# Kernel tuning notes

Measured on AMD Instinct MI355X. Metric: run time of the kernel, lower is better.

The kernel has to match this reference:

```python
import jax, jax.numpy as jnp
import numpy as np

B, N, ND = 4096, 28, 3        # batch, nodes (2 hands x 14 joints), xyz
ED, DD = 512, 256             # encoder dim, decoder dim
H, DH = 8, 64                 # heads, dim_head (inner = 512)
EDEPTH, DDEPTH = 2, 1
EMLP, DMLP = 4 * ED, 4 * DD
NM = 14                       # num_masked = int(0.5 * 28)


def _ln(x, s, b):
    m = jnp.mean(x, -1, keepdims=True)
    v = jnp.var(x, -1, keepdims=True)
    return (x - m) * jax.lax.rsqrt(v + 1e-5) * s + b


def _transformer(x, a, ln1_s, ln1_b, Wqkv, Wo, bo, ln2_s, ln2_b, W1, b1, W2, b2):
    # pre-norm transformer; adjacency a [b,n,n] enters as an additive attention bias
    b, n, _ = x.shape
    scale = DH ** -0.5
    for i in range(ln1_s.shape[0]):
        h = _ln(x, ln1_s[i], ln1_b[i])
        q, k, v = jnp.split(h @ Wqkv[i], 3, axis=-1)
        q = q.reshape(b, n, H, DH).transpose(0, 2, 1, 3)
        k = k.reshape(b, n, H, DH).transpose(0, 2, 1, 3)
        v = v.reshape(b, n, H, DH).transpose(0, 2, 1, 3)
        dots = jnp.einsum('bhid,bhjd->bhij', q, k) * scale + a[:, None]
        attn = jax.nn.softmax(dots, axis=-1)
        o = jnp.einsum('bhij,bhjd->bhid', attn, v).transpose(0, 2, 1, 3).reshape(b, n, H * DH)
        x = x + o @ Wo[i] + bo[i]
        h2 = _ln(x, ln2_s[i], ln2_b[i])
        x = x + jax.nn.gelu(h2 @ W1[i] + b1[i]) @ W2[i] + b2[i]
    return x


def setup_inputs() -> dict:
    key = jax.random.key(0)
    ks = iter(jax.random.split(key, 40))
    nrm = lambda shp, s=0.02: jax.random.normal(next(ks), shp, dtype=jnp.float32) * s
    x = jax.random.normal(next(ks), (B, N, ND), dtype=jnp.float32)
    a = jax.random.uniform(next(ks), (B, N, N), dtype=jnp.float32)
    perm = jnp.argsort(jax.random.uniform(next(ks), (B, N)), axis=-1).astype(jnp.int32)
    masked_indices, unmasked_indices = perm[:, :NM], perm[:, NM:]
    inp = dict(x=x, a=a, masked_indices=masked_indices, unmasked_indices=unmasked_indices)
    inp.update(
        W_emb=nrm((ND, ED)), b_emb=jnp.zeros((ED,), jnp.float32), pos_emb=nrm((N, ED), 0.02),
        e_ln1_s=jnp.ones((EDEPTH, ED)), e_ln1_b=jnp.zeros((EDEPTH, ED)),
        e_Wqkv=nrm((EDEPTH, ED, 3 * H * DH)), e_Wo=nrm((EDEPTH, H * DH, ED)), e_bo=jnp.zeros((EDEPTH, ED)),
        e_ln2_s=jnp.ones((EDEPTH, ED)), e_ln2_b=jnp.zeros((EDEPTH, ED)),
        e_W1=nrm((EDEPTH, ED, EMLP)), e_b1=jnp.zeros((EDEPTH, EMLP)),
        e_W2=nrm((EDEPTH, EMLP, ED)), e_b2=jnp.zeros((EDEPTH, ED)),
        enc2dec_W=nrm((ED, DD)), enc2dec_b=jnp.zeros((DD,), jnp.float32),
        mask_token=nrm((DD,), 1.0), dec_pos_emb=nrm((N, DD), 0.02),
        d_ln1_s=jnp.ones((DDEPTH, DD)), d_ln1_b=jnp.zeros((DDEPTH, DD)),
        d_Wqkv=nrm((DDEPTH, DD, 3 * H * DH)), d_Wo=nrm((DDEPTH, H * DH, DD)), d_bo=jnp.zeros((DDEPTH, DD)),
        d_ln2_s=jnp.ones((DDEPTH, DD)), d_ln2_b=jnp.zeros((DDEPTH, DD)),
        d_W1=nrm((DDEPTH, DD, DMLP)), d_b1=jnp.zeros((DDEPTH, DMLP)),
        d_W2=nrm((DDEPTH, DMLP, DD)), d_b2=jnp.zeros((DDEPTH, DD)),
        pred_W=nrm((DD, ND)), pred_b=jnp.zeros((ND,), jnp.float32),
    )
    return inp


def reference(x, a, masked_indices, unmasked_indices,
              W_emb, b_emb, pos_emb,
              e_ln1_s, e_ln1_b, e_Wqkv, e_Wo, e_bo, e_ln2_s, e_ln2_b, e_W1, e_b1, e_W2, e_b2,
              enc2dec_W, enc2dec_b, mask_token, dec_pos_emb,
              d_ln1_s, d_ln1_b, d_Wqkv, d_Wo, d_bo, d_ln2_s, d_ln2_b, d_W1, d_b1, d_W2, d_b2,
              pred_W, pred_b):
    # node embedding (1x1 conv over nodes == per-node linear) + positional embedding
    tokens = x @ W_emb + b_emb + pos_emb                                   # [B,N,ED]
    unm_tok = jnp.take_along_axis(tokens, unmasked_indices[:, :, None], axis=1)  # [B,N-NM,ED]
    masked_nodes = jnp.take_along_axis(x, masked_indices[:, :, None], axis=1)    # [B,NM,ND]
    # batched adjacency slicing (replaces the per-sample python loop in torch)
    unmasked_a = jax.vmap(lambda ai, ii: ai[ii[:, None], ii[None, :]])(a, unmasked_indices)
    enc = _transformer(unm_tok, unmasked_a,
                       e_ln1_s, e_ln1_b, e_Wqkv, e_Wo, e_bo, e_ln2_s, e_ln2_b, e_W1, e_b1, e_W2, e_b2)
    dec_tok = enc @ enc2dec_W + enc2dec_b                                  # [B,N-NM,DD]
    mask_toks = mask_token + dec_pos_emb[masked_indices]                   # [B,NM,DD]
    # NOTE: faithful to original: unmasked pos-emb tokens are computed but NOT used in the cat
    decoder_tokens = jnp.concatenate([mask_toks, dec_tok], axis=1)         # [B,N,DD]
    decoded = _transformer(decoder_tokens, a,
                           d_ln1_s, d_ln1_b, d_Wqkv, d_Wo, d_bo, d_ln2_s, d_ln2_b, d_W1, d_b1, d_W2, d_b2)
    mt = jnp.take_along_axis(decoded, masked_indices[:, :, None], axis=1)  # [B,NM,DD]
    masked_pred = mt @ pred_W + pred_b                                     # [B,NM,ND]
    recon_loss = jnp.mean((masked_pred - masked_nodes) ** 2)
    return (decoder_tokens, masked_nodes, masked_indices, masked_pred, recon_loss)
```

## Files before the change

kernel.cpp:

```cpp
#include <hip/hip_runtime.h>
#include <math.h>

#define B_TOT 4096
#define N_SEQ 28
#define NDIM 3
#define ED 512
#define DD 256
#define NH 8
#define DHD 64
#define EMLP 2048
#define DMLP 1024
#define NM 14
#define NU 14

typedef __attribute__((ext_vector_type(8))) short short8;
typedef __attribute__((ext_vector_type(4))) float f32x4;
typedef unsigned short ushort_t;
typedef unsigned int uint_t;

__device__ __forceinline__ float gelu_f(float x) {
    float x3 = x * x * x;
    return 0.5f * x * (1.0f + tanhf(0.7978845608028654f * (x + 0.044715f * x3)));
}
__device__ __forceinline__ ushort_t f2bf(float f) {
    union { float f; uint_t u; } c; c.f = f;
    uint_t u = c.u;
    return (ushort_t)((u + 0x7FFFu + ((u >> 16) & 1u)) >> 16);
}
__device__ __forceinline__ float bf2f(ushort_t h) {
    union { uint_t u; float f; } c; c.u = ((uint_t)h) << 16;
    return c.f;
}
__device__ __forceinline__ float bf_lo(uint_t u) {
    union { uint_t u; float f; } c; c.u = u << 16;
    return c.f;
}
__device__ __forceinline__ float bf_hi(uint_t u) {
    union { uint_t u; float f; } c; c.u = u & 0xFFFF0000u;
    return c.f;
}
__device__ __forceinline__ void gl_lds16(const ushort_t* g, ushort_t* l) {
    __builtin_amdgcn_global_load_lds(
        (const __attribute__((address_space(1))) unsigned int*)g,
        (__attribute__((address_space(3))) unsigned int*)l, 16, 0, 0);
}

__global__ void k_zero(float* p) { p[threadIdx.x] = 0.0f; }
__global__ void k_final(const float* acc, float* out) {
    out[0] = acc[0] * (1.0f / (float)(B_TOT * NM * NDIM));
}

__global__ void k_wconv(const float* __restrict__ W, ushort_t* __restrict__ Wt, int K, int N) {
    __shared__ float tile[32][33];
    int n0 = blockIdx.x * 32, k0 = blockIdx.y * 32;
    int tr = threadIdx.x >> 5, tc = threadIdx.x & 31;
#pragma unroll
    for (int i = 0; i < 4; ++i)
        tile[tr + i * 8][tc] = W[(size_t)(k0 + tr + i * 8) * N + n0 + tc];
    __syncthreads();
#pragma unroll
    for (int i = 0; i < 4; ++i)
        Wt[(size_t)(n0 + tr + i * 8) * K + k0 + tc] = f2bf(tile[tc][tr + i * 8]);
}

__global__ void k_embed(const float* __restrict__ x, const float* __restrict__ a,
                        const int* __restrict__ mi, const int* __restrict__ ui,
                        const float* __restrict__ W_emb, const float* __restrict__ b_emb,
                        const float* __restrict__ pos_emb,
                        ushort_t* __restrict__ X, float* __restrict__ ua,
                        float* __restrict__ out_mn, float* __restrict__ out_midx,
                        int base) {
    int s = blockIdx.x;
    int g = base + s;
    int t = threadIdx.x;
    for (int i = 0; i < NU; ++i) {
        int u = ui[g * NU + i];
        float x0 = x[((size_t)g * N_SEQ + u) * NDIM + 0];
        float x1 = x[((size_t)g * N_SEQ + u) * NDIM + 1];
        float x2 = x[((size_t)g * N_SEQ + u) * NDIM + 2];
        for (int d = t; d < ED; d += 256) {
            X[((size_t)s * NU + i) * ED + d] = f2bf(
                x0 * W_emb[d] + x1 * W_emb[ED + d] + x2 * W_emb[2 * ED + d]
                + b_emb[d] + pos_emb[(size_t)u * ED + d]);
        }
    }
    for (int idx = t; idx < NU * NU; idx += 256) {
        int i = idx / NU, j = idx % NU;
        int uii = ui[g * NU + i], ujj = ui[g * NU + j];
        ua[(size_t)s * NU * NU + idx] = a[(size_t)g * N_SEQ * N_SEQ + (size_t)uii * N_SEQ + ujj];
    }
    for (int idx = t; idx < NM * NDIM; idx += 256) {
        int i = idx / NDIM, c = idx % NDIM;
        int m = mi[g * NM + i];
        out_mn[((size_t)g * NM + i) * NDIM + c] = x[((size_t)g * N_SEQ + m) * NDIM + c];
    }
    for (int i = t; i < NM; i += 256) {
        out_midx[(size_t)g * NM + i] = (float)mi[g * NM + i];
    }
}

template <int D>
__global__ void k_ln(const ushort_t* __restrict__ in, ushort_t* __restrict__ out,
                     const float* __restrict__ sc, const float* __restrict__ bi, int M) {
    int wave = threadIdx.x >> 6;
    int lane = threadIdx.x & 63;
    int row = blockIdx.x * 4 + wave;
    if (row >= M) return;
    constexpr int PL = D / 64;
    const ushort_t* rp = in + (size_t)row * D + lane * PL;
    uint_t u[PL / 2];
    if (PL == 8) *(uint4*)u = *(const uint4*)rp;
    else *(uint2*)u = *(const uint2*)rp;
    float v[PL];
    float sum = 0.f, sq = 0.f;
#pragma unroll
    for (int q = 0; q < PL / 2; ++q) {
        v[2 * q] = bf_lo(u[q]);
        v[2 * q + 1] = bf_hi(u[q]);
    }
#pragma unroll
    for (int j = 0; j < PL; ++j) { sum += v[j]; sq += v[j] * v[j]; }
#pragma unroll
    for (int o = 32; o >= 1; o >>= 1) {
        sum += __shfl_xor(sum, o);
        sq += __shfl_xor(sq, o);
    }
    float mean = sum * (1.0f / D);
    float var = sq * (1.0f / D) - mean * mean;
    float r = rsqrtf(var + 1e-5f);
    uint_t w[PL / 2];
#pragma unroll
    for (int q = 0; q < PL / 2; ++q) {
        int d = lane * PL + 2 * q;
        float a0 = (v[2 * q] - mean) * r * sc[d] + bi[d];
        float a1 = (v[2 * q + 1] - mean) * r * sc[d + 1] + bi[d + 1];
        w[q] = (uint_t)f2bf(a0) | ((uint_t)f2bf(a1) << 16);
    }
    ushort_t* op = out + (size_t)row * D + lane * PL;
    if (PL == 8) *(uint4*)op = *(uint4*)w;
    else *(uint2*)op = *(uint2*)w;
}

template <int ACT, int OM, int NTv>
__global__ __launch_bounds__(256) void k_gemm_mfma(
    const ushort_t* __restrict__ A, const ushort_t* __restrict__ Wt,
    const float* __restrict__ bias, const ushort_t* __restrict__ res,
    ushort_t* __restrict__ Cout, ushort_t* __restrict__ VTout, int M, int N, int K) {
    __shared__ ushort_t As[128 * 32];
    __shared__ ushort_t Bs[128 * 32];
    const int t = threadIdx.x;
    const int gx = gridDim.x;
    int flat = blockIdx.y * gx + blockIdx.x;
    int nwg = gx * gridDim.y;
    int q8 = nwg >> 3, r8 = nwg & 7;
    int xcd = flat & 7, loc = flat >> 3;
    int wg = (xcd < r8 ? xcd * (q8 + 1) : r8 * (q8 + 1) + (xcd - r8) * q8) + loc;
    const int bm = wg / gx, bn = wg % gx;

    const int lane = t & 63;
    const int wave = t >> 6;
    const int wr = wave >> 1, wc = wave & 1;
    const int l15 = lane & 15;
    const int kg = (lane >> 4) * 8;

    const int srow = wave * 32 + (lane >> 2);
    const int scol = (lane & 3) * 8;
    const ushort_t* Ag = A + (size_t)(bm * 128 + srow) * K + scol;
    const ushort_t* Bg = Wt + (size_t)(bn * 128 + srow) * K + scol;
    ushort_t* Al0 = &As[(wave * 32) * 32];
    ushort_t* Al1 = &As[(wave * 32 + 16) * 32];
    ushort_t* Bl0 = &Bs[(wave * 32) * 32];
    ushort_t* Bl1 = &Bs[(wave * 32 + 16) * 32];

    f32x4 acc[4][4] = {};

    for (int k0 = 0; k0 < K; k0 += 32) {
        gl_lds16(Ag + k0, Al0);
        gl_lds16(Ag + (size_t)16 * K + k0, Al1);
        gl_lds16(Bg + k0, Bl0);
        gl_lds16(Bg + (size_t)16 * K + k0, Bl1);
        __syncthreads();
        short8 af[4], bfr[4];
#pragma unroll
        for (int m = 0; m < 4; ++m)
            af[m] = *(const short8*)&As[(wr * 64 + m * 16 + l15) * 32 + kg];
#pragma unroll
        for (int n = 0; n < 4; ++n)
            bfr[n] = *(const short8*)&Bs[(wc * 64 + n * 16 + l15) * 32 + kg];
#pragma unroll
        for (int m = 0; m < 4; ++m)
#pragma unroll
            for (int n = 0; n < 4; ++n)
                acc[m][n] = __builtin_amdgcn_mfma_f32_16x16x32_bf16(af[m], bfr[n], acc[m][n], 0, 0, 0);
        __syncthreads();
    }

    const int crow0 = bm * 128 + wr * 64;
    const int ccol0 = bn * 128 + wc * 64;
#pragma unroll
    for (int m = 0; m < 4; ++m) {
#pragma unroll
        for (int n = 0; n < 4; ++n) {
            int col = ccol0 + n * 16 + l15;
            float bv = bias ? bias[col] : 0.0f;
#pragma unroll
            for (int r = 0; r < 4; ++r) {
                int row = crow0 + m * 16 + (lane >> 4) * 4 + r;
                float v = acc[m][n][r] + bv;
                if (res) v += bf2f(res[(size_t)row * N + col]);
                if (ACT == 1) v = gelu_f(v);
                if (OM == 2) {
                    if (col < 1024) {
                        Cout[(size_t)row * 1536 + col] = f2bf(v);
                    } else {
                        int sq = row / NTv, ntok = row - sq * NTv;
                        int d = col & 63, hh = (col - 1024) >> 6;
                        VTout[(((size_t)sq * 8 + hh) * 64 + d) * 32 + ntok] = f2bf(v);
                    }
                } else {
                    Cout[(size_t)row * N + col] = f2bf(v);
                }
            }
        }
    }
}

template <int NT>
__global__ __launch_bounds__(256) void k_attn_mfma(
    const ushort_t* __restrict__ qkv, const ushort_t* __restrict__ vt,
    const float* __restrict__ bias, ushort_t* __restrict__ O) {
    constexpr int NTP = (NT + 15) & ~15;
    constexpr int MT = NTP / 16;
    constexpr int QS = 72;
    constexpr int VS = 40;
    __shared__ __align__(16) ushort_t smem[4 * NTP * QS * 2 + 4 * 64 * VS];
    ushort_t* Qs = smem;
    ushort_t* Ks = smem + 4 * NTP * QS;
    ushort_t* Vs = Ks + 4 * NTP * QS;
    ushort_t* Ps = smem;

    const int s = blockIdx.x, hg = blockIdx.y;
    const int t = threadIdx.x;
    const int wave = t >> 6, lane = t & 63;
    const int l15 = lane & 15, g4 = lane >> 4;

    const ushort_t* qb = qkv + (size_t)s * NT * 1536 + hg * 256;
    for (int c = t; c < 64 * NT; c += 256) {
        int c8 = c & 7;
        int rem = c >> 3;
        int r = rem % NT;
        int ph = rem / NT;
        int h = ph & 3, p = ph >> 2;
        uint4 v = *(const uint4*)(qb + (size_t)r * 1536 + p * 512 + h * 64 + c8 * 8);
        ushort_t* dst = (p ? Ks : Qs) + (h * NTP + r) * QS + c8 * 8;
        *(uint4*)dst = v;
    }
    const ushort_t* vb = vt + ((size_t)s * 8 + hg * 4) * 64 * 32;
    for (int c = t; c < 4 * 64 * 4; c += 256) {
        int n8 = c & 3;
        int d = (c >> 2) & 63;
        int h = c >> 8;
        uint4 v = *(const uint4*)(vb + (size_t)(h * 64 + d) * 32 + n8 * 8);
        uint_t* pv = (uint_t*)&v;
#pragma unroll
        for (int q = 0; q < 4; ++q) {
            int cc = n8 * 8 + q * 2;
            if (cc >= NT) pv[q] = 0;
            else if (cc + 1 >= NT) pv[q] &= 0xFFFFu;
        }
        *(uint4*)&Vs[(h * 64 + d) * VS + n8 * 8] = v;
    }
    __syncthreads();

    const int h = wave;
    const ushort_t* Qh = Qs + h * NTP * QS;
    const ushort_t* Kh = Ks + h * NTP * QS;
    const ushort_t* Vh = Vs + h * 64 * VS;
    ushort_t* Ph = Ps + h * NTP * VS;

    f32x4 sacc[MT][MT] = {};
#pragma unroll
    for (int ks = 0; ks < 2; ++ks) {
        short8 qf[MT], kf[MT];
#pragma unroll
        for (int m = 0; m < MT; ++m)
            qf[m] = *(const short8*)&Qh[(m * 16 + l15) * QS + ks * 32 + g4 * 8];
#pragma unroll
        for (int n = 0; n < MT; ++n)
            kf[n] = *(const short8*)&Kh[(n * 16 + l15) * QS + ks * 32 + g4 * 8];
#pragma unroll
        for (int m = 0; m < MT; ++m)
#pragma unroll
            for (int n = 0; n < MT; ++n)
                sacc[m][n] = __builtin_amdgcn_mfma_f32_16x16x32_bf16(qf[m], kf[n], sacc[m][n], 0, 0, 0);
    }

    const float* bp = bias + (size_t)s * NT * NT;
    float prv[MT][MT][4];
#pragma unroll
    for (int m = 0; m < MT; ++m) {
#pragma unroll
        for (int r = 0; r < 4; ++r) {
            int i = m * 16 + g4 * 4 + r;
            float sv[MT];
#pragma unroll
            for (int n = 0; n < MT; ++n) {
                int j = n * 16 + l15;
                sv[n] = (i < NT && j < NT) ? sacc[m][n][r] * 0.125f + bp[i * NT + j] : -1e30f;
            }
            float mx = sv[0];
            if (MT > 1) mx = fmaxf(mx, sv[MT - 1]);
#pragma unroll
            for (int o = 1; o < 16; o <<= 1) mx = fmaxf(mx, __shfl_xor(mx, o));
            float sum = 0.f;
#pragma unroll
            for (int n = 0; n < MT; ++n) {
                float e = (sv[n] > -1e29f) ? __expf(sv[n] - mx) : 0.f;
                prv[m][n][r] = e;
                sum += e;
            }
#pragma unroll
            for (int o = 1; o < 16; o <<= 1) sum += __shfl_xor(sum, o);
            float rs = sum > 0.f ? 1.0f / sum : 0.f;
#pragma unroll
            for (int n = 0; n < MT; ++n) prv[m][n][r] *= rs;
        }
    }
    __syncthreads();

    if (NTP == 16) {
        for (int z = lane; z < 16 * 8; z += 64) {
            int i = z >> 3, jw = z & 7;
            *(uint_t*)&Ph[i * VS + 16 + jw * 2] = 0;
        }
    }
#pragma unroll
    for (int m = 0; m < MT; ++m)
#pragma unroll
        for (int n = 0; n < MT; ++n)
#pragma unroll
            for (int r = 0; r < 4; ++r)
                Ph[(m * 16 + g4 * 4 + r) * VS + n * 16 + l15] = f2bf(prv[m][n][r]);
    __syncthreads();

    f32x4 oacc[MT][4] = {};
    {
        short8 pf[MT], vf[4];
#pragma unroll
        for (int m = 0; m < MT; ++m)
            pf[m] = *(const short8*)&Ph[(m * 16 + l15) * VS + g4 * 8];
#pragma unroll
        for (int nd = 0; nd < 4; ++nd)
            vf[nd] = *(const short8*)&Vh[(nd * 16 + l15) * VS + g4 * 8];
#pragma unroll
        for (int m = 0; m < MT; ++m)
#pragma unroll
            for (int nd = 0; nd < 4; ++nd)
                oacc[m][nd] = __builtin_amdgcn_mfma_f32_16x16x32_bf16(pf[m], vf[nd], oacc[m][nd], 0, 0, 0);
    }

    ushort_t* Ob = O + (size_t)s * NT * 512 + hg * 256 + h * 64;
#pragma unroll
    for (int m = 0; m < MT; ++m)
#pragma unroll
        for (int r = 0; r < 4; ++r) {
            int i = m * 16 + g4 * 4 + r;
            if (i < NT) {
#pragma unroll
                for (int nd = 0; nd < 4; ++nd)
                    Ob[(size_t)i * 512 + nd * 16 + l15] = f2bf(oacc[m][nd][r]);
            }
        }
}

__global__ void k_build_dec(const ushort_t* __restrict__ dec_tok, const float* __restrict__ mask_token,
                            const float* __restrict__ dec_pos, const int* __restrict__ mi,
                            ushort_t* __restrict__ Xd, float* __restrict__ out0, int base) {
    int s = blockIdx.x;
    int g = base + s;
    int t = threadIdx.x;
    for (int idx = t; idx < N_SEQ * DD; idx += 256) {
        int i = idx / DD, d = idx % DD;
        float v;
        if (i < NM) {
            int m = mi[g * NM + i];
            v = mask_token[d] + dec_pos[(size_t)m * DD + d];
        } else {
            v = bf2f(dec_tok[((size_t)s * NU + (i - NM)) * DD + d]);
        }
        Xd[((size_t)s * N_SEQ + i) * DD + d] = f2bf(v);
        out0[((size_t)g * N_SEQ + i) * DD + d] = v;
    }
}

__global__ void k_pred(const ushort_t* __restrict__ Xd, const int* __restrict__ mi,
                       const float* __restrict__ pW, const float* __restrict__ pb,
                       const float* __restrict__ mn, float* __restrict__ out_pred,
                       float* __restrict__ loss, int base, int Bc) {
    int tid = blockIdx.x * 256 + threadIdx.x;
    int total = Bc * NM * NDIM;
    float part = 0.f;
    if (tid < total) {
        int c = tid % NDIM;
        int r = tid / NDIM;
        int i = r % NM;
        int s = r / NM;
        int g = base + s;
        int m = mi[g * NM + i];
        const ushort_t* row = Xd + ((size_t)s * N_SEQ + m) * DD;
        float acc = pb[c];
        for (int k = 0; k < DD; ++k) acc += bf2f(row[k]) * pW[k * NDIM + c];
        out_pred[((size_t)g * NM + i) * NDIM + c] = acc;
        float d = acc - mn[((size_t)g * NM + i) * NDIM + c];
        part = d * d;
    }
    __shared__ float red[256];
    red[threadIdx.x] = part;
    __syncthreads();
    for (int o = 128; o > 0; o >>= 1) {
        if (threadIdx.x < o) red[threadIdx.x] += red[threadIdx.x + o];
        __syncthreads();
    }
    if (threadIdx.x == 0) atomicAdd(loss, red[0]);
}

extern "C" void kernel_launch(void* const* d_in, const int* in_sizes, int n_in,
                              void* d_out, int out_size, void* d_ws, size_t ws_size,
                              hipStream_t stream) {
    const float* x       = (const float*)d_in[0];
    const float* a       = (const float*)d_in[1];
    const int*   mi      = (const int*)d_in[2];
    const int*   ui      = (const int*)d_in[3];
    const float* W_emb   = (const float*)d_in[4];
    const float* b_emb   = (const float*)d_in[5];
    const float* pos_emb = (const float*)d_in[6];
    const float* e_ln1_s = (const float*)d_in[7];
    const float* e_ln1_b = (const float*)d_in[8];
    const float* e_Wqkv  = (const float*)d_in[9];
    const float* e_Wo    = (const float*)d_in[10];
    const float* e_bo    = (const float*)d_in[11];
    const float* e_ln2_s = (const float*)d_in[12];
    const float* e_ln2_b = (const float*)d_in[13];
    const float* e_W1    = (const float*)d_in[14];
    const float* e_b1    = (const float*)d_in[15];
    const float* e_W2    = (const float*)d_in[16];
    const float* e_b2    = (const float*)d_in[17];
    const float* e2d_W   = (const float*)d_in[18];
    const float* e2d_b   = (const float*)d_in[19];
    const float* mask_tok= (const float*)d_in[20];
    const float* dec_pos = (const float*)d_in[21];
    const float* d_ln1_s = (const float*)d_in[22];
    const float* d_ln1_b = (const float*)d_in[23];
    const float* d_Wqkv  = (const float*)d_in[24];
    const float* d_Wo    = (const float*)d_in[25];
    const float* d_bo    = (const float*)d_in[26];
    const float* d_ln2_s = (const float*)d_in[27];
    const float* d_ln2_b = (const float*)d_in[28];
    const float* d_W1    = (const float*)d_in[29];
    const float* d_b1    = (const float*)d_in[30];
    const float* d_W2    = (const float*)d_in[31];
    const float* d_b2    = (const float*)d_in[32];
    const float* pred_W  = (const float*)d_in[33];
    const float* pred_b  = (const float*)d_in[34];

    float* out0 = (float*)d_out;
    float* out1 = out0 + (size_t)B_TOT * N_SEQ * DD;
    float* out2 = out1 + (size_t)B_TOT * NM * NDIM;
    float* out3 = out2 + (size_t)B_TOT * NM;
    float* out4 = out3 + (size_t)B_TOT * NM * NDIM;

    char* wp = (char*)d_ws;
    size_t off = 0;
    auto alloc = [&](size_t bytes) {
        size_t o = off;
        off = (off + bytes + 255) & ~(size_t)255;
        return (void*)(wp + o);
    };
    float* loss_acc = (float*)alloc(64 * 4);
    ushort_t* wt_eqkv = (ushort_t*)alloc((size_t)2 * 1536 * 512 * 2);
    ushort_t* wt_ewo  = (ushort_t*)alloc((size_t)2 * 512 * 512 * 2);
    ushort_t* wt_ew1  = (ushort_t*)alloc((size_t)2 * 2048 * 512 * 2);
    ushort_t* wt_ew2  = (ushort_t*)alloc((size_t)2 * 512 * 2048 * 2);
    ushort_t* wt_dqkv = (ushort_t*)alloc((size_t)1536 * 256 * 2);
    ushort_t* wt_dwo  = (ushort_t*)alloc((size_t)256 * 512 * 2);
    ushort_t* wt_dw1  = (ushort_t*)alloc((size_t)1024 * 256 * 2);
    ushort_t* wt_dw2  = (ushort_t*)alloc((size_t)256 * 1024 * 2);
    ushort_t* wt_e2d  = (ushort_t*)alloc((size_t)256 * 512 * 2);
    size_t fixed_bytes = off;

    const size_t per_seq = 2 * (7168 + 3584 + 7168 + 43008 + 14336 + 16384) + 4 * 196;
    int Bc = B_TOT;
    while (Bc > 64 && fixed_bytes + (size_t)Bc * per_seq + 8192 > ws_size) Bc >>= 1;

    ushort_t* Xbuf   = (ushort_t*)alloc((size_t)Bc * 7168 * 2);
    ushort_t* Dbuf   = (ushort_t*)alloc((size_t)Bc * 3584 * 2);
    float*    uabuf  = (float*)alloc((size_t)Bc * 196 * 4);
    ushort_t* Hbuf   = (ushort_t*)alloc((size_t)Bc * 7168 * 2);
    ushort_t* QKVbuf = (ushort_t*)alloc((size_t)Bc * 43008 * 2);
    ushort_t* Obuf   = (ushort_t*)alloc((size_t)Bc * 14336 * 2);
    ushort_t* VTbuf  = (ushort_t*)alloc((size_t)Bc * 16384 * 2);

    k_zero<<<1, 64, 0, stream>>>(loss_acc);

    for (int l = 0; l < 2; ++l) {
        k_wconv<<<dim3(1536 / 32, 512 / 32), 256, 0, stream>>>(e_Wqkv + (size_t)l * 512 * 1536, wt_eqkv + (size_t)l * 1536 * 512, 512, 1536);
        k_wconv<<<dim3(512 / 32, 512 / 32), 256, 0, stream>>>(e_Wo + (size_t)l * 512 * 512, wt_ewo + (size_t)l * 512 * 512, 512, 512);
        k_wconv<<<dim3(2048 / 32, 512 / 32), 256, 0, stream>>>(e_W1 + (size_t)l * 512 * 2048, wt_ew1 + (size_t)l * 2048 * 512, 512, 2048);
        k_wconv<<<dim3(512 / 32, 2048 / 32), 256, 0, stream>>>(e_W2 + (size_t)l * 2048 * 512, wt_ew2 + (size_t)l * 512 * 2048, 2048, 512);
    }
    k_wconv<<<dim3(1536 / 32, 256 / 32), 256, 0, stream>>>(d_Wqkv, wt_dqkv, 256, 1536);
    k_wconv<<<dim3(256 / 32, 512 / 32), 256, 0, stream>>>(d_Wo, wt_dwo, 512, 256);
    k_wconv<<<dim3(1024 / 32, 256 / 32), 256, 0, stream>>>(d_W1, wt_dw1, 256, 1024);
    k_wconv<<<dim3(256 / 32, 1024 / 32), 256, 0, stream>>>(d_W2, wt_dw2, 1024, 256);
    k_wconv<<<dim3(256 / 32, 512 / 32), 256, 0, stream>>>(e2d_W, wt_e2d, 512, 256);

    const int nchunk = B_TOT / Bc;
    for (int c = 0; c < nchunk; ++c) {
        int base = c * Bc;
        int M = Bc * NU;
        int Md = Bc * N_SEQ;

        k_embed<<<Bc, 256, 0, stream>>>(x, a, mi, ui, W_emb, b_emb, pos_emb,
                                        Xbuf, uabuf, out1, out2, base);
        for (int l = 0; l < 2; ++l) {
            k_ln<ED><<<M / 4, 256, 0, stream>>>(Xbuf, Hbuf, e_ln1_s + l * ED, e_ln1_b + l * ED, M);
            k_gemm_mfma<0, 2, NU><<<dim3(1536 / 128, M / 128), 256, 0, stream>>>(
                Hbuf, wt_eqkv + (size_t)l * 1536 * 512, nullptr, nullptr, QKVbuf, VTbuf, M, 1536, ED);
            k_attn_mfma<NU><<<dim3(Bc, 2), 256, 0, stream>>>(QKVbuf, VTbuf, uabuf, Obuf);
            k_gemm_mfma<0, 1, 1><<<dim3(ED / 128, M / 128), 256, 0, stream>>>(
                Obuf, wt_ewo + (size_t)l * 512 * 512, e_bo + l * ED, Xbuf, Xbuf, nullptr, M, ED, 512);
            k_ln<ED><<<M / 4, 256, 0, stream>>>(Xbuf, Hbuf, e_ln2_s + l * ED, e_ln2_b + l * ED, M);
            k_gemm_mfma<1, 1, 1><<<dim3(EMLP / 128, M / 128), 256, 0, stream>>>(
                Hbuf, wt_ew1 + (size_t)l * 2048 * 512, e_b1 + l * EMLP, nullptr, QKVbuf, nullptr, M, EMLP, ED);
            k_gemm_mfma<0, 1, 1><<<dim3(ED / 128, M / 128), 256, 0, stream>>>(
                QKVbuf, wt_ew2 + (size_t)l * 512 * 2048, e_b2 + l * ED, Xbuf, Xbuf, nullptr, M, ED, EMLP);
        }
        k_gemm_mfma<0, 1, 1><<<dim3(DD / 128, M / 128), 256, 0, stream>>>(
            Xbuf, wt_e2d, e2d_b, nullptr, Dbuf, nullptr, M, DD, ED);
        k_build_dec<<<Bc, 256, 0, stream>>>(Dbuf, mask_tok, dec_pos, mi, Xbuf, out0, base);
        k_ln<DD><<<Md / 4, 256, 0, stream>>>(Xbuf, Hbuf, d_ln1_s, d_ln1_b, Md);
        k_gemm_mfma<0, 2, N_SEQ><<<dim3(1536 / 128, Md / 128), 256, 0, stream>>>(
            Hbuf, wt_dqkv, nullptr, nullptr, QKVbuf, VTbuf, Md, 1536, DD);
        k_attn_mfma<N_SEQ><<<dim3(Bc, 2), 256, 0, stream>>>(QKVbuf, VTbuf, a + (size_t)base * N_SEQ * N_SEQ, Obuf);
        k_gemm_mfma<0, 1, 1><<<dim3(DD / 128, Md / 128), 256, 0, stream>>>(
            Obuf, wt_dwo, d_bo, Xbuf, Xbuf, nullptr, Md, DD, 512);
        k_ln<DD><<<Md / 4, 256, 0, stream>>>(Xbuf, Hbuf, d_ln2_s, d_ln2_b, Md);
        k_gemm_mfma<1, 1, 1><<<dim3(DMLP / 128, Md / 128), 256, 0, stream>>>(
            Hbuf, wt_dw1, d_b1, nullptr, QKVbuf, nullptr, Md, DMLP, DD);
        k_gemm_mfma<0, 1, 1><<<dim3(DD / 128, Md / 128), 256, 0, stream>>>(
            QKVbuf, wt_dw2, d_b2, Xbuf, Xbuf, nullptr, Md, DD, DMLP);
        int tot = Bc * NM * NDIM;
        k_pred<<<(tot + 255) / 256, 256, 0, stream>>>(
            Xbuf, mi, pred_W, pred_b, out1, out3, loss_acc, base, Bc);
    }
    k_final<<<1, 1, 0, stream>>>(loss_acc, out4);
}
```

Baseline: 3.288 ms.

## Double-buffer GEMM LDS loads, stage epilogue through LDS, drop V-transpose buffer

The MFMA GEMM now double-buffers its A/B LDS tiles so the next K-slice's global-to-LDS copy overlaps the current slice's MFMAs, using explicit vmcnt waits and barriers. The epilogue writes the accumulators to LDS and then does row-contiguous 16-byte loads and stores for bias, residual and GELU, where it previously did scattered 2-byte accesses. The separate transposed-V output path is removed; attention transposes V from the QKV buffer into LDS itself, which saves a global buffer and some write traffic. GELU uses an exp-based tanh. The epilogue now rounds accumulators to bf16 before adding bias and residual, which adds a little numeric error.

```diff
diff --git a/kernel.cpp b/kernel.cpp
--- a/kernel.cpp
+++ b/kernel.cpp
@@ -19,8 +19,10 @@
 typedef unsigned int uint_t;
 
 __device__ __forceinline__ float gelu_f(float x) {
-    float x3 = x * x * x;
-    return 0.5f * x * (1.0f + tanhf(0.7978845608028654f * (x + 0.044715f * x3)));
+    float t = 0.7978845608028654f * (x + 0.044715f * x * x * x);
+    float e = __expf(2.0f * t);
+    float th = 1.0f - 2.0f / (e + 1.0f);
+    return 0.5f * x * (1.0f + th);
 }
 __device__ __forceinline__ ushort_t f2bf(float f) {
     union { float f; uint_t u; } c; c.f = f;
@@ -141,13 +143,17 @@
     else *(uint2*)op = *(uint2*)w;
 }
 
-template <int ACT, int OM, int NTv>
+template <int ACT>
 __global__ __launch_bounds__(256) void k_gemm_mfma(
     const ushort_t* __restrict__ A, const ushort_t* __restrict__ Wt,
     const float* __restrict__ bias, const ushort_t* __restrict__ res,
-    ushort_t* __restrict__ Cout, ushort_t* __restrict__ VTout, int M, int N, int K) {
-    __shared__ ushort_t As[128 * 32];
-    __shared__ ushort_t Bs[128 * 32];
+    ushort_t* __restrict__ Cout, int M, int N, int K) {
+    __shared__ __align__(16) ushort_t smem[17408];
+    ushort_t* As0 = smem;
+    ushort_t* As1 = smem + 4096;
+    ushort_t* Bs0 = smem + 8192;
+    ushort_t* Bs1 = smem + 12288;
+
     const int t = threadIdx.x;
     const int gx = gridDim.x;
     int flat = blockIdx.y * gx + blockIdx.x;
@@ -161,74 +167,113 @@
     const int wave = t >> 6;
     const int wr = wave >> 1, wc = wave & 1;
     const int l15 = lane & 15;
-    const int kg = (lane >> 4) * 8;
+    const int g4 = lane >> 4;
+    const int kg = g4 * 8;
 
     const int srow = wave * 32 + (lane >> 2);
     const int scol = (lane & 3) * 8;
     const ushort_t* Ag = A + (size_t)(bm * 128 + srow) * K + scol;
     const ushort_t* Bg = Wt + (size_t)(bn * 128 + srow) * K + scol;
-    ushort_t* Al0 = &As[(wave * 32) * 32];
-    ushort_t* Al1 = &As[(wave * 32 + 16) * 32];
-    ushort_t* Bl0 = &Bs[(wave * 32) * 32];
-    ushort_t* Bl1 = &Bs[(wave * 32 + 16) * 32];
+    const int wb0 = (wave * 32) * 32;
+    const int wb1 = (wave * 32 + 16) * 32;
 
     f32x4 acc[4][4] = {};
-
-    for (int k0 = 0; k0 < K; k0 += 32) {
-        gl_lds16(Ag + k0, Al0);
-        gl_lds16(Ag + (size_t)16 * K + k0, Al1);
-        gl_lds16(Bg + k0, Bl0);
-        gl_lds16(Bg + (size_t)16 * K + k0, Bl1);
-        __syncthreads();
+    const int nt = K >> 5;
+
+    gl_lds16(Ag, As0 + wb0);
+    gl_lds16(Ag + (size_t)16 * K, As0 + wb1);
+    gl_lds16(Bg, Bs0 + wb0);
+    gl_lds16(Bg + (size_t)16 * K, Bs0 + wb1);
+
+    for (int tt = 0; tt < nt; ++tt) {
+        ushort_t* Ac = (tt & 1) ? As1 : As0;
+        ushort_t* Bc = (tt & 1) ? Bs1 : Bs0;
+        if (tt + 1 < nt) {
+            int k0 = (tt + 1) << 5;
+            ushort_t* An = (tt & 1) ? As0 : As1;
+            ushort_t* Bn = (tt & 1) ? Bs0 : Bs1;
+            gl_lds16(Ag + k0, An + wb0);
+            gl_lds16(Ag + (size_t)16 * K + k0, An + wb1);
+            gl_lds16(Bg + k0, Bn + wb0);
+            gl_lds16(Bg + (size_t)16 * K + k0, Bn + wb1);
+            asm volatile("s_waitcnt vmcnt(4)" ::: "memory");
+        } else {
+            asm volatile("s_waitcnt vmcnt(0)" ::: "memory");
+        }
+        __builtin_amdgcn_s_barrier();
+        __builtin_amdgcn_sched_barrier(0);
         short8 af[4], bfr[4];
 #pragma unroll
         for (int m = 0; m < 4; ++m)
-            af[m] = *(const short8*)&As[(wr * 64 + m * 16 + l15) * 32 + kg];
+            af[m] = *(const short8*)&Ac[(wr * 64 + m * 16 + l15) * 32 + kg];
 #pragma unroll
         for (int n = 0; n < 4; ++n)
-            bfr[n] = *(const short8*)&Bs[(wc * 64 + n * 16 + l15) * 32 + kg];
+            bfr[n] = *(const short8*)&Bc[(wc * 64 + n * 16 + l15) * 32 + kg];
 #pragma unroll
         for (int m = 0; m < 4; ++m)
 #pragma unroll
             for (int n = 0; n < 4; ++n)
                 acc[m][n] = __builtin_amdgcn_mfma_f32_16x16x32_bf16(af[m], bfr[n], acc[m][n], 0, 0, 0);
-        __syncthreads();
-    }
-
-    const int crow0 = bm * 128 + wr * 64;
-    const int ccol0 = bn * 128 + wc * 64;
-#pragma unroll
-    for (int m = 0; m < 4; ++m) {
-#pragma unroll
-        for (int n = 0; n < 4; ++n) {
-            int col = ccol0 + n * 16 + l15;
-            float bv = bias ? bias[col] : 0.0f;
+        __builtin_amdgcn_sched_barrier(0);
+        __builtin_amdgcn_s_barrier();
+    }
+
+    ushort_t* Cs = smem;
+    const int erow0 = wr * 64, ecol0 = wc * 64;
+#pragma unroll
+    for (int m = 0; m < 4; ++m)
+#pragma unroll
+        for (int n = 0; n < 4; ++n)
 #pragma unroll
             for (int r = 0; r < 4; ++r) {
-                int row = crow0 + m * 16 + (lane >> 4) * 4 + r;
-                float v = acc[m][n][r] + bv;
-                if (res) v += bf2f(res[(size_t)row * N + col]);
-                if (ACT == 1) v = gelu_f(v);
-                if (OM == 2) {
-                    if (col < 1024) {
-                        Cout[(size_t)row * 1536 + col] = f2bf(v);
-                    } else {
-                        int sq = row / NTv, ntok = row - sq * NTv;
-                        int d = col & 63, hh = (col - 1024) >> 6;
-                        VTout[(((size_t)sq * 8 + hh) * 64 + d) * 32 + ntok] = f2bf(v);
-                    }
-                } else {
-                    Cout[(size_t)row * N + col] = f2bf(v);
+                float v = acc[m][n][r];
+                float o = __shfl_xor(v, 1);
+                if (!(l15 & 1)) {
+                    uint_t pk = (uint_t)f2bf(v) | ((uint_t)f2bf(o) << 16);
+                    *(uint_t*)&Cs[(erow0 + m * 16 + g4 * 4 + r) * 136 + ecol0 + n * 16 + l15] = pk;
                 }
             }
-        }
+    __builtin_amdgcn_s_barrier();
+
+    const int row = t >> 1, half = t & 1;
+    const int grow = bm * 128 + row;
+    const int gc0 = bn * 128 + half * 64;
+    const ushort_t* rres = res ? res + (size_t)grow * N + gc0 : (const ushort_t*)0;
+    ushort_t* gout = Cout + (size_t)grow * N + gc0;
+#pragma unroll
+    for (int c = 0; c < 8; ++c) {
+        uint4 pv = *(const uint4*)&Cs[row * 136 + half * 64 + c * 8];
+        uint_t* pw = (uint_t*)&pv;
+        float vv[8];
+#pragma unroll
+        for (int q = 0; q < 4; ++q) { vv[2 * q] = bf_lo(pw[q]); vv[2 * q + 1] = bf_hi(pw[q]); }
+        if (bias) {
+#pragma unroll
+            for (int j = 0; j < 8; ++j) vv[j] += bias[gc0 + c * 8 + j];
+        }
+        if (res) {
+            uint4 rv = *(const uint4*)(rres + c * 8);
+            uint_t* pr = (uint_t*)&rv;
+#pragma unroll
+            for (int q = 0; q < 4; ++q) { vv[2 * q] += bf_lo(pr[q]); vv[2 * q + 1] += bf_hi(pr[q]); }
+        }
+        if (ACT == 1) {
+#pragma unroll
+            for (int j = 0; j < 8; ++j) vv[j] = gelu_f(vv[j]);
+        }
+        uint4 ov;
+        uint_t* po = (uint_t*)&ov;
+#pragma unroll
+        for (int q = 0; q < 4; ++q)
+            po[q] = (uint_t)f2bf(vv[2 * q]) | ((uint_t)f2bf(vv[2 * q + 1]) << 16);
+        *(uint4*)(gout + c * 8) = ov;
     }
 }
 
 template <int NT>
 __global__ __launch_bounds__(256) void k_attn_mfma(
-    const ushort_t* __restrict__ qkv, const ushort_t* __restrict__ vt,
-    const float* __restrict__ bias, ushort_t* __restrict__ O) {
+    const ushort_t* __restrict__ qkv, const float* __restrict__ bias,
+    ushort_t* __restrict__ O) {
     constexpr int NTP = (NT + 15) & ~15;
     constexpr int MT = NTP / 16;
     constexpr int QS = 72;
@@ -255,20 +300,23 @@
         ushort_t* dst = (p ? Ks : Qs) + (h * NTP + r) * QS + c8 * 8;
         *(uint4*)dst = v;
     }
-    const ushort_t* vb = vt + ((size_t)s * 8 + hg * 4) * 64 * 32;
-    for (int c = t; c < 4 * 64 * 4; c += 256) {
-        int n8 = c & 3;
-        int d = (c >> 2) & 63;
-        int h = c >> 8;
-        uint4 v = *(const uint4*)(vb + (size_t)(h * 64 + d) * 32 + n8 * 8);
-        uint_t* pv = (uint_t*)&v;
-#pragma unroll
-        for (int q = 0; q < 4; ++q) {
-            int cc = n8 * 8 + q * 2;
-            if (cc >= NT) pv[q] = 0;
-            else if (cc + 1 >= NT) pv[q] &= 0xFFFFu;
-        }
-        *(uint4*)&Vs[(h * 64 + d) * VS + n8 * 8] = v;
+    const ushort_t* vrow = qkv + (size_t)s * NT * 1536 + 1024 + hg * 256;
+    for (int c = t; c < 4 * 64 * (32 - NT); c += 256) {
+        int p = c % (32 - NT);
+        int hd = c / (32 - NT);
+        Vs[hd * VS + NT + p] = 0;
+    }
+    for (int c = t; c < 4 * NT * 8; c += 256) {
+        int c8 = c & 7;
+        int r = (c >> 3) % NT;
+        int h = (c >> 3) / NT;
+        uint4 v = *(const uint4*)(vrow + (size_t)r * 1536 + h * 64 + c8 * 8);
+        const uint_t* pv = (const uint_t*)&v;
+#pragma unroll
+        for (int j = 0; j < 4; ++j) {
+            Vs[(h * 64 + c8 * 8 + 2 * j) * VS + r] = (ushort_t)(pv[j] & 0xFFFFu);
+            Vs[(h * 64 + c8 * 8 + 2 * j + 1) * VS + r] = (ushort_t)(pv[j] >> 16);
+        }
     }
     __syncthreads();
 
@@ -488,7 +536,7 @@
     ushort_t* wt_e2d  = (ushort_t*)alloc((size_t)256 * 512 * 2);
     size_t fixed_bytes = off;
 
-    const size_t per_seq = 2 * (7168 + 3584 + 7168 + 43008 + 14336 + 16384) + 4 * 196;
+    const size_t per_seq = 2 * (7168 + 3584 + 7168 + 43008 + 14336) + 4 * 196;
     int Bc = B_TOT;
     while (Bc > 64 && fixed_bytes + (size_t)Bc * per_seq + 8192 > ws_size) Bc >>= 1;
 
@@ -498,7 +546,6 @@
     ushort_t* Hbuf   = (ushort_t*)alloc((size_t)Bc * 7168 * 2);
     ushort_t* QKVbuf = (ushort_t*)alloc((size_t)Bc * 43008 * 2);
     ushort_t* Obuf   = (ushort_t*)alloc((size_t)Bc * 14336 * 2);
-    ushort_t* VTbuf  = (ushort_t*)alloc((size_t)Bc * 16384 * 2);
 
     k_zero<<<1, 64, 0, stream>>>(loss_acc);
 
@@ -524,31 +571,31 @@
                                         Xbuf, uabuf, out1, out2, base);
         for (int l = 0; l < 2; ++l) {
             k_ln<ED><<<M / 4, 256, 0, stream>>>(Xbuf, Hbuf, e_ln1_s + l * ED, e_ln1_b + l * ED, M);
-            k_gemm_mfma<0, 2, NU><<<dim3(1536 / 128, M / 128), 256, 0, stream>>>(
-                Hbuf, wt_eqkv + (size_t)l * 1536 * 512, nullptr, nullptr, QKVbuf, VTbuf, M, 1536, ED);
-            k_attn_mfma<NU><<<dim3(Bc, 2), 256, 0, stream>>>(QKVbuf, VTbuf, uabuf, Obuf);
-            k_gemm_mfma<0, 1, 1><<<dim3(ED / 128, M / 128), 256, 0, stream>>>(
-                Obuf, wt_ewo + (size_t)l * 512 * 512, e_bo + l * ED, Xbuf, Xbuf, nullptr, M, ED, 512);
+            k_gemm_mfma<0><<<dim3(1536 / 128, M / 128), 256, 0, stream>>>(
+                Hbuf, wt_eqkv + (size_t)l * 1536 * 512, nullptr, nullptr, QKVbuf, M, 1536, ED);
+            k_attn_mfma<NU><<<dim3(Bc, 2), 256, 0, stream>>>(QKVbuf, uabuf, Obuf);
+            k_gemm_mfma<0><<<dim3(ED / 128, M / 128), 256, 0, stream>>>(
+                Obuf, wt_ewo + (size_t)l * 512 * 512, e_bo + l * ED, Xbuf, Xbuf, M, ED, 512);
             k_ln<ED><<<M / 4, 256, 0, stream>>>(Xbuf, Hbuf, e_ln2_s + l * ED, e_ln2_b + l * ED, M);
-            k_gemm_mfma<1, 1, 1><<<dim3(EMLP / 128, M / 128), 256, 0, stream>>>(
-                Hbuf, wt_ew1 + (size_t)l * 2048 * 512, e_b1 + l * EMLP, nullptr, QKVbuf, nullptr, M, EMLP, ED);
-            k_gemm_mfma<0, 1, 1><<<dim3(ED / 128, M / 128), 256, 0, stream>>>(
-                QKVbuf, wt_ew2 + (size_t)l * 512 * 2048, e_b2 + l * ED, Xbuf, Xbuf, nullptr, M, ED, EMLP);
-        }
-        k_gemm_mfma<0, 1, 1><<<dim3(DD / 128, M / 128), 256, 0, stream>>>(
-            Xbuf, wt_e2d, e2d_b, nullptr, Dbuf, nullptr, M, DD, ED);
+            k_gemm_mfma<1><<<dim3(EMLP / 128, M / 128), 256, 0, stream>>>(
+                Hbuf, wt_ew1 + (size_t)l * 2048 * 512, e_b1 + l * EMLP, nullptr, QKVbuf, M, EMLP, ED);
+            k_gemm_mfma<0><<<dim3(ED / 128, M / 128), 256, 0, stream>>>(
+                QKVbuf, wt_ew2 + (size_t)l * 512 * 2048, e_b2 + l * ED, Xbuf, Xbuf, M, ED, EMLP);
+        }
+        k_gemm_mfma<0><<<dim3(DD / 128, M / 128), 256, 0, stream>>>(
+            Xbuf, wt_e2d, e2d_b, nullptr, Dbuf, M, DD, ED);
         k_build_dec<<<Bc, 256, 0, stream>>>(Dbuf, mask_tok, dec_pos, mi, Xbuf, out0, base);
         k_ln<DD><<<Md / 4, 256, 0, stream>>>(Xbuf, Hbuf, d_ln1_s, d_ln1_b, Md);
-        k_gemm_mfma<0, 2, N_SEQ><<<dim3(1536 / 128, Md / 128), 256, 0, stream>>>(
-            Hbuf, wt_dqkv, nullptr, nullptr, QKVbuf, VTbuf, Md, 1536, DD);
-        k_attn_mfma<N_SEQ><<<dim3(Bc, 2), 256, 0, stream>>>(QKVbuf, VTbuf, a + (size_t)base * N_SEQ * N_SEQ, Obuf);
-        k_gemm_mfma<0, 1, 1><<<dim3(DD / 128, Md / 128), 256, 0, stream>>>(
-            Obuf, wt_dwo, d_bo, Xbuf, Xbuf, nullptr, Md, DD, 512);
+        k_gemm_mfma<0><<<dim3(1536 / 128, Md / 128), 256, 0, stream>>>(
+            Hbuf, wt_dqkv, nullptr, nullptr, QKVbuf, Md, 1536, DD);
+        k_attn_mfma<N_SEQ><<<dim3(Bc, 2), 256, 0, stream>>>(QKVbuf, a + (size_t)base * N_SEQ * N_SEQ, Obuf);
+        k_gemm_mfma<0><<<dim3(DD / 128, Md / 128), 256, 0, stream>>>(
+            Obuf, wt_dwo, d_bo, Xbuf, Xbuf, Md, DD, 512);
         k_ln<DD><<<Md / 4, 256, 0, stream>>>(Xbuf, Hbuf, d_ln2_s, d_ln2_b, Md);
-        k_gemm_mfma<1, 1, 1><<<dim3(DMLP / 128, Md / 128), 256, 0, stream>>>(
-            Hbuf, wt_dw1, d_b1, nullptr, QKVbuf, nullptr, Md, DMLP, DD);
-        k_gemm_mfma<0, 1, 1><<<dim3(DD / 128, Md / 128), 256, 0, stream>>>(
-            QKVbuf, wt_dw2, d_b2, Xbuf, Xbuf, nullptr, Md, DD, DMLP);
+        k_gemm_mfma<1><<<dim3(DMLP / 128, Md / 128), 256, 0, stream>>>(
+            Hbuf, wt_dw1, d_b1, nullptr, QKVbuf, Md, DMLP, DD);
+        k_gemm_mfma<0><<<dim3(DD / 128, Md / 128), 256, 0, stream>>>(
+            QKVbuf, wt_dw2, d_b2, Xbuf, Xbuf, Md, DD, DMLP);
         int tot = Bc * NM * NDIM;
         k_pred<<<(tot + 255) / 256, 256, 0, stream>>>(
             Xbuf, mi, pred_W, pred_b, out1, out3, loss_acc, base, Bc);
```

Measured after the change: 2.845 ms. -13.5%, faster.
